# Performance work log

Hardware: AMD Instinct MI355X
Metric: run time of the kernel (lower is better)

## Reference

```python
import jax, jax.numpy as jnp
import numpy as np

ROUTINGS = 4
NUM_CAPSULE = 16
DIM_CAPSULE = 16
EPS = 1e-7  # K.epsilon()
L2_EPS = 1e-12  # tf.nn.l2_normalize epsilon


def squash(x, axis=-1):
    s = jnp.sum(jnp.square(x), axis=axis, keepdims=True) + EPS
    scale = jnp.sqrt(s) / (0.5 + s)
    return scale * x


def l2_normalize(x, axis=-1):
    s = jnp.sum(jnp.square(x), axis=axis, keepdims=True)
    return x * jax.lax.rsqrt(jnp.maximum(s, L2_EPS))


def setup_inputs() -> dict:
    key = jax.random.key(0)
    k1, k2 = jax.random.split(key)
    u_vecs = jax.random.normal(k1, (32, 4096, 128), dtype=jnp.float32)
    # glorot-ish scale for kernel-size-1 conv weight (input_dim=128 -> num_cap*dim_cap=256)
    W = jax.random.normal(k2, (128, 256), dtype=jnp.float32) * 0.05
    return {"u_vecs": u_vecs, "W": W}


def reference(u_vecs, W):
    B, I, _ = u_vecs.shape
    # conv1d with kernel size 1 == pointwise projection
    u_hat = jnp.einsum('bid,dk->bik', u_vecs, W)
    u_hat = u_hat.reshape(B, I, NUM_CAPSULE, DIM_CAPSULE)
    u_hat = jnp.transpose(u_hat, (0, 2, 1, 3))  # [B, N, I, D]

    b = jnp.zeros((B, NUM_CAPSULE, I), dtype=u_hat.dtype)
    o = None
    for i in range(ROUTINGS):
        c = jax.nn.softmax(b, axis=1)  # softmax over output-capsule axis
        o = jnp.einsum('bni,bnid->bnd', c, u_hat)  # [B, N, D]
        if i < ROUTINGS - 1:
            o = l2_normalize(o, axis=-1)
            b = jnp.einsum('bnd,bnid->bni', o, u_hat)  # logits reset each iter
    return squash(o, axis=-1)
```

## Files before the change

### kernel.cpp

```cpp
#include <hip/hip_runtime.h>

#define BATCH 32
#define I_TOT 4096
#define N_CAP 16
#define K_DIM 128
#define RCHUNK 128
#define NCHUNK 32
#define CCHUNK 64
#define NCHUNK_CS 64

#define WS_WO    0
#define WS_SP    65536
#define WS_PACK  2162688
#define WS_PACKT (WS_PACK + 8388608)
#define WS_TOTAL_F (WS_PACKT + 8388608)

typedef __attribute__((ext_vector_type(8))) short bf16x8;
typedef __attribute__((ext_vector_type(4))) float f32x4;

__device__ inline ushort f2bf(float x) {
    unsigned u = __float_as_uint(x);
    u += 0x7FFFu + ((u >> 16) & 1u);
    return (ushort)(u >> 16);
}

__global__ __launch_bounds__(256) void pack_kernel(const float* __restrict__ u,
                                                   float* __restrict__ ws, int do_pack) {
    const int b = blockIdx.y, chunk = blockIdx.x, t = threadIdx.x;
    const int c0 = chunk * CCHUNK;
    ushort* up = (ushort*)(ws + WS_PACK);
    ushort* ut = (ushort*)(ws + WS_PACKT);
    const int k4 = t & 31, rg = t >> 5;

    __shared__ ushort lds_bf[CCHUNK][K_DIM + 8];
    __shared__ __align__(16) float4 red[8][32];

    float4 acc = {0.f, 0.f, 0.f, 0.f};
    #pragma unroll
    for (int m = 0; m < 8; m++) {
        int R = c0 + m * 8 + rg;
        float4 v = *(const float4*)&u[((size_t)b * I_TOT + R) * K_DIM + k4 * 4];
        acc.x += v.x; acc.y += v.y; acc.z += v.z; acc.w += v.w;
        if (do_pack) {
            ushort4 w = { f2bf(v.x), f2bf(v.y), f2bf(v.z), f2bf(v.w) };
            int k = k4 * 4;
            int kt = k >> 5, lane_hi = (k & 31) >> 3, j0 = k & 7;
            size_t off = (((size_t)(b * 256 + (R >> 4)) * 4 + kt) * 64
                          + (R & 15) + (lane_hi << 4)) * 8 + j0;
            *(ushort4*)&up[off] = w;
            *(ushort4*)&lds_bf[m * 8 + rg][k] = w;
        }
    }
    red[rg][k4] = acc;
    __syncthreads();
    if (t < 32) {
        float4 s = red[0][t];
        #pragma unroll
        for (int r = 1; r < 8; r++) {
            float4 v = red[r][t];
            s.x += v.x; s.y += v.y; s.z += v.z; s.w += v.w;
        }
        *(float4*)&ws[WS_SP + ((size_t)(b * NCHUNK_CS + chunk)) * K_DIM + t * 4] = s;
    }

    if (do_pack) {
        __syncthreads();
        #pragma unroll
        for (int q = 0; q < 4; q++) {
            int cc = q * 256 + t;
            int k = cc & 127, io = cc >> 7;
            int ig0 = c0 + io * 8;
            bf16x8 w8;
            #pragma unroll
            for (int j = 0; j < 8; j++) w8[j] = (short)lds_bf[io * 8 + j][k];
            size_t off = ((((size_t)(b * 8 + (k >> 4))) * 128 + (ig0 >> 5)) * 64
                          + (k & 15) + ((io & 3) << 4)) * 8;
            *(bf16x8*)&ut[off] = w8;
        }
    }
}

__global__ __launch_bounds__(128) void update_kernel(const float* __restrict__ W,
                                                     float* __restrict__ ws,
                                                     float* __restrict__ out,
                                                     int mode) {
    const int n = blockIdx.x, b = blockIdx.y, t = threadIdx.x;

    __shared__ float s_n[K_DIM];
    __shared__ float o_s[N_CAP + 4];

    if (mode == 0) {
        const float* sp = ws + WS_SP + (size_t)b * NCHUNK_CS * K_DIM;
        float a = 0.f;
        #pragma unroll 8
        for (int c = 0; c < NCHUNK_CS; c++) a += sp[(size_t)c * K_DIM + t];
        s_n[t] = a * (1.f / 16.f);
    } else {
        const float* sp = ws + WS_SP + (size_t)b * NCHUNK * 2048 + n * K_DIM;
        float a = 0.f;
        #pragma unroll 8
        for (int c = 0; c < NCHUNK; c++) a += sp[(size_t)c * 2048 + t];
        s_n[t] = a;
    }
    __syncthreads();

    {
        const int d = t >> 3, kseg = t & 7;
        const int col = n * 16 + d;
        float p = 0.f;
        #pragma unroll
        for (int j = 0; j < 16; j++) {
            int k = kseg * 16 + j;
            p += s_n[k] * W[k * 256 + col];
        }
        p += __shfl_xor(p, 1); p += __shfl_xor(p, 2); p += __shfl_xor(p, 4);
        if (kseg == 0) o_s[d] = p;
    }
    __syncthreads();

    float ss = (mode == 2) ? 1e-7f : 0.f;
    #pragma unroll
    for (int d = 0; d < 16; d++) { float v = o_s[d]; ss += v * v; }

    if (mode == 2) {
        if (t < 16) {
            float scale = sqrtf(ss) / (0.5f + ss);
            out[b * 256 + n * 16 + t] = scale * o_s[t];
        }
        return;
    }

    const float inv = rsqrtf(fmaxf(ss, 1e-12f));
    const float4* wrow = (const float4*)(W + t * 256 + n * 16);
    const float4* o4 = (const float4*)o_s;
    float acc = 0.f;
    #pragma unroll
    for (int q = 0; q < 4; q++) {
        float4 w = wrow[q];
        float4 o = o4[q];
        acc += w.x * o.x + w.y * o.y + w.z * o.z + w.w * o.w;
    }
    ws[WS_WO + (size_t)b * 2048 + n * K_DIM + t] = acc * inv;
}

__global__ __launch_bounds__(256) void routing_mfma(float* __restrict__ ws) {
    const int b = blockIdx.y, chunk = blockIdx.x, t = threadIdx.x;
    const int lane = t & 63, wave = t >> 6;
    const short* up = (const short*)(ws + WS_PACK);
    const short* utp = (const short*)(ws + WS_PACKT);

    __shared__ __align__(16) short wo_bf[N_CAP][144];
    __shared__ float c_s[RCHUNK][18];

    const float* wo = ws + WS_WO + (size_t)b * 2048;
    #pragma unroll
    for (int j = 0; j < 8; j++) {
        int idx = t + j * 256;
        wo_bf[idx >> 7][idx & 127] = (short)f2bf(wo[idx]);
    }
    __syncthreads();

    const int cap = lane & 15, hi = lane >> 4;
    bf16x8 bfrag[4];
    #pragma unroll
    for (int kt = 0; kt < 4; kt++)
        bfrag[kt] = *(const bf16x8*)&wo_bf[cap][kt * 32 + hi * 8];

    #pragma unroll
    for (int rr = 0; rr < 2; rr++) {
        const int rt = wave * 2 + rr;
        const int rt_g = chunk * 8 + rt;
        f32x4 acc = {0.f, 0.f, 0.f, 0.f};
        const short* abase = up + (((size_t)(b * 256 + rt_g)) * 4) * 512 + lane * 8;
        #pragma unroll
        for (int kt = 0; kt < 4; kt++) {
            bf16x8 a = *(const bf16x8*)(abase + kt * 512);
            acc = __builtin_amdgcn_mfma_f32_16x16x32_bf16(a, bfrag[kt], acc, 0, 0, 0);
        }
        #pragma unroll
        for (int r = 0; r < 4; r++) {
            float v = acc[r];
            float mx = v;
            mx = fmaxf(mx, __shfl_xor(mx, 1)); mx = fmaxf(mx, __shfl_xor(mx, 2));
            mx = fmaxf(mx, __shfl_xor(mx, 4)); mx = fmaxf(mx, __shfl_xor(mx, 8));
            float e = __expf(v - mx);
            float sm = e;
            sm += __shfl_xor(sm, 1); sm += __shfl_xor(sm, 2);
            sm += __shfl_xor(sm, 4); sm += __shfl_xor(sm, 8);
            c_s[rt * 16 + hi * 4 + r][cap] = e / sm;
        }
    }
    __syncthreads();

    f32x4 s0 = {0.f, 0.f, 0.f, 0.f}, s1 = {0.f, 0.f, 0.f, 0.f};
    const size_t ut_b = ((size_t)b * 8) * 128;
    #pragma unroll
    for (int ic = 0; ic < 4; ic++) {
        bf16x8 bfr;
        #pragma unroll
        for (int j = 0; j < 8; j++)
            bfr[j] = (short)f2bf(c_s[ic * 32 + hi * 8 + j][cap]);
        const short* ab0 = utp + (((ut_b + (size_t)(wave * 2 + 0) * 128) + chunk * 4 + ic) * 64 + lane) * 8;
        const short* ab1 = utp + (((ut_b + (size_t)(wave * 2 + 1) * 128) + chunk * 4 + ic) * 64 + lane) * 8;
        bf16x8 a0 = *(const bf16x8*)ab0;
        bf16x8 a1 = *(const bf16x8*)ab1;
        s0 = __builtin_amdgcn_mfma_f32_16x16x32_bf16(a0, bfr, s0, 0, 0, 0);
        s1 = __builtin_amdgcn_mfma_f32_16x16x32_bf16(a1, bfr, s1, 0, 0, 0);
    }
    float* sp = ws + WS_SP + ((size_t)b * NCHUNK + chunk) * 2048;
    #pragma unroll
    for (int r = 0; r < 4; r++) {
        sp[cap * K_DIM + (wave * 2 + 0) * 16 + hi * 4 + r] = s0[r];
        sp[cap * K_DIM + (wave * 2 + 1) * 16 + hi * 4 + r] = s1[r];
    }
}

__global__ __launch_bounds__(256) void routing_fp32(const float* __restrict__ u,
                                                    float* __restrict__ ws) {
    const int b = blockIdx.y, chunk = blockIdx.x, t = threadIdx.x;
    const int i0 = chunk * RCHUNK;

    __shared__ __align__(16) float wo_s[N_CAP][K_DIM];
    __shared__ __align__(16) float c_s[RCHUNK][N_CAP];

    const float* w_o = ws + WS_WO + (size_t)b * 2048;
    #pragma unroll
    for (int j = 0; j < 8; j++) {
        int idx = t + j * 256;
        ((float*)wo_s)[idx] = w_o[idx];
    }
    __syncthreads();

    {
        const int row = t >> 1, h = t & 1;
        const float4* upx = (const float4*)(u + ((size_t)b * I_TOT + i0 + row) * K_DIM + h * 64);
        const float4* wp = (const float4*)&wo_s[0][h * 64];
        float logit[16];
        #pragma unroll
        for (int n = 0; n < 16; n++) logit[n] = 0.f;
        #pragma unroll
        for (int q = 0; q < 16; q++) {
            float4 v = upx[q];
            #pragma unroll
            for (int n = 0; n < 16; n++) {
                float4 w = wp[n * 32 + q];
                logit[n] += v.x * w.x + v.y * w.y + v.z * w.z + v.w * w.w;
            }
        }
        #pragma unroll
        for (int n = 0; n < 16; n++) logit[n] += __shfl_xor(logit[n], 1);
        float m = logit[0];
        #pragma unroll
        for (int n = 1; n < 16; n++) m = fmaxf(m, logit[n]);
        float sum = 0.f;
        #pragma unroll
        for (int n = 0; n < 16; n++) { logit[n] = __expf(logit[n] - m); sum += logit[n]; }
        float inv = 1.f / sum;
        float4* crow = (float4*)&c_s[row][h * 8];
        if (h == 0) {
            crow[0] = make_float4(logit[0]*inv, logit[1]*inv, logit[2]*inv, logit[3]*inv);
            crow[1] = make_float4(logit[4]*inv, logit[5]*inv, logit[6]*inv, logit[7]*inv);
        } else {
            crow[0] = make_float4(logit[8]*inv, logit[9]*inv, logit[10]*inv, logit[11]*inv);
            crow[1] = make_float4(logit[12]*inv, logit[13]*inv, logit[14]*inv, logit[15]*inv);
        }
    }
    __syncthreads();

    const int k4 = t & 31, ng = t >> 5;
    float4 a0 = {0.f,0.f,0.f,0.f}, a1 = {0.f,0.f,0.f,0.f};
    const float4* u2 = (const float4*)(u + ((size_t)b * I_TOT + i0) * K_DIM) + k4;
    #pragma unroll 8
    for (int i = 0; i < RCHUNK; i++) {
        float4 v = u2[(size_t)i * 32];
        float2 c2 = *(const float2*)&c_s[i][ng * 2];
        a0.x += v.x * c2.x; a0.y += v.y * c2.x; a0.z += v.z * c2.x; a0.w += v.w * c2.x;
        a1.x += v.x * c2.y; a1.y += v.y * c2.y; a1.z += v.z * c2.y; a1.w += v.w * c2.y;
    }
    float* sp = ws + WS_SP + ((size_t)b * NCHUNK + chunk) * 2048;
    *(float4*)&sp[(ng * 2 + 0) * K_DIM + k4 * 4] = a0;
    *(float4*)&sp[(ng * 2 + 1) * K_DIM + k4 * 4] = a1;
}

extern "C" void kernel_launch(void* const* d_in, const int* in_sizes, int n_in,
                              void* d_out, int out_size, void* d_ws, size_t ws_size,
                              hipStream_t stream) {
    const float* u = (const float*)d_in[0];
    const float* W = (const float*)d_in[1];
    float* out = (float*)d_out;
    float* ws = (float*)d_ws;

    const int big = (ws_size >= (size_t)WS_TOTAL_F * 4) ? 1 : 0;

    pack_kernel<<<dim3(I_TOT / CCHUNK, BATCH), 256, 0, stream>>>(u, ws, big);
    update_kernel<<<dim3(N_CAP, BATCH), 128, 0, stream>>>(W, ws, out, 0);

    for (int pass = 0; pass < 3; pass++) {
        if (big) routing_mfma<<<dim3(NCHUNK, BATCH), 256, 0, stream>>>(ws);
        else     routing_fp32<<<dim3(NCHUNK, BATCH), 256, 0, stream>>>(u, ws);
        update_kernel<<<dim3(N_CAP, BATCH), 128, 0, stream>>>(W, ws, out, pass == 2 ? 2 : 1);
    }
}
```

Before: 84.04 us.

## Fuse capsule update into routing kernel and double the per-block row chunk

Each routing block now reduces the previous pass's partial sums itself, projects them through W, normalizes, and builds the bf16 weighted-W tile, so the separate update kernel launches go away. Partial sums are double-buffered in the workspace so that this in-block reduction can read the prior pass while the current pass writes. The chunk size grows to 256 rows for both pack and routing, halving the grid and the number of partials. A small final kernel applies squash. The cost is that every block redundantly repeats the reduction and W projection for its batch, and the grid has fewer blocks.

```diff
diff --git a/kernel.cpp b/kernel.cpp
--- a/kernel.cpp
+++ b/kernel.cpp
@@ -4,16 +4,20 @@
 #define I_TOT 4096
 #define N_CAP 16
 #define K_DIM 128
-#define RCHUNK 128
-#define NCHUNK 32
-#define CCHUNK 64
-#define NCHUNK_CS 64
-
-#define WS_WO    0
+
+#define PCHUNK 256
+#define NPCH   16
+
+#define WS_CS    0
 #define WS_SP    65536
-#define WS_PACK  2162688
+#define WS_PACK  (WS_SP + 2097152)
 #define WS_PACKT (WS_PACK + 8388608)
 #define WS_TOTAL_F (WS_PACKT + 8388608)
+
+#define FB_WO   WS_PACK
+#define FB_SP   (WS_PACK + 65536)
+#define FB_NCHUNK 32
+#define RCHUNK 128
 
 typedef __attribute__((ext_vector_type(8))) short bf16x8;
 typedef __attribute__((ext_vector_type(4))) float f32x4;
@@ -27,28 +31,47 @@
 __global__ __launch_bounds__(256) void pack_kernel(const float* __restrict__ u,
                                                    float* __restrict__ ws, int do_pack) {
     const int b = blockIdx.y, chunk = blockIdx.x, t = threadIdx.x;
-    const int c0 = chunk * CCHUNK;
+    const int c0 = chunk * PCHUNK;
     ushort* up = (ushort*)(ws + WS_PACK);
     ushort* ut = (ushort*)(ws + WS_PACKT);
     const int k4 = t & 31, rg = t >> 5;
 
-    __shared__ ushort lds_bf[CCHUNK][K_DIM + 8];
+    __shared__ ushort lds_bf[64][K_DIM + 8];
     __shared__ __align__(16) float4 red[8][32];
 
     float4 acc = {0.f, 0.f, 0.f, 0.f};
-    #pragma unroll
-    for (int m = 0; m < 8; m++) {
-        int R = c0 + m * 8 + rg;
-        float4 v = *(const float4*)&u[((size_t)b * I_TOT + R) * K_DIM + k4 * 4];
-        acc.x += v.x; acc.y += v.y; acc.z += v.z; acc.w += v.w;
+    for (int slab = 0; slab < 4; slab++) {
+        const int s0 = c0 + slab * 64;
+        #pragma unroll
+        for (int m = 0; m < 8; m++) {
+            int R = s0 + m * 8 + rg;
+            float4 v = *(const float4*)&u[((size_t)b * I_TOT + R) * K_DIM + k4 * 4];
+            acc.x += v.x; acc.y += v.y; acc.z += v.z; acc.w += v.w;
+            if (do_pack) {
+                ushort4 w = { f2bf(v.x), f2bf(v.y), f2bf(v.z), f2bf(v.w) };
+                int k = k4 * 4;
+                int kt = k >> 5, lane_hi = (k & 31) >> 3, j0 = k & 7;
+                size_t off = (((size_t)(b * 256 + (R >> 4)) * 4 + kt) * 64
+                              + (R & 15) + (lane_hi << 4)) * 8 + j0;
+                *(ushort4*)&up[off] = w;
+                *(ushort4*)&lds_bf[m * 8 + rg][k] = w;
+            }
+        }
         if (do_pack) {
-            ushort4 w = { f2bf(v.x), f2bf(v.y), f2bf(v.z), f2bf(v.w) };
-            int k = k4 * 4;
-            int kt = k >> 5, lane_hi = (k & 31) >> 3, j0 = k & 7;
-            size_t off = (((size_t)(b * 256 + (R >> 4)) * 4 + kt) * 64
-                          + (R & 15) + (lane_hi << 4)) * 8 + j0;
-            *(ushort4*)&up[off] = w;
-            *(ushort4*)&lds_bf[m * 8 + rg][k] = w;
+            __syncthreads();
+            #pragma unroll
+            for (int q = 0; q < 4; q++) {
+                int cc = q * 256 + t;
+                int k = cc & 127, io = cc >> 7;
+                int ig0 = s0 + io * 8;
+                bf16x8 w8;
+                #pragma unroll
+                for (int j = 0; j < 8; j++) w8[j] = (short)lds_bf[io * 8 + j][k];
+                size_t off = ((((size_t)(b * 8 + (k >> 4))) * 128 + (ig0 >> 5)) * 64
+                              + (k & 15) + ((io & 3) << 4)) * 8;
+                *(bf16x8*)&ut[off] = w8;
+            }
+            __syncthreads();
         }
     }
     red[rg][k4] = acc;
@@ -60,103 +83,78 @@
             float4 v = red[r][t];
             s.x += v.x; s.y += v.y; s.z += v.z; s.w += v.w;
         }
-        *(float4*)&ws[WS_SP + ((size_t)(b * NCHUNK_CS + chunk)) * K_DIM + t * 4] = s;
-    }
-
-    if (do_pack) {
-        __syncthreads();
-        #pragma unroll
-        for (int q = 0; q < 4; q++) {
-            int cc = q * 256 + t;
-            int k = cc & 127, io = cc >> 7;
-            int ig0 = c0 + io * 8;
-            bf16x8 w8;
-            #pragma unroll
-            for (int j = 0; j < 8; j++) w8[j] = (short)lds_bf[io * 8 + j][k];
-            size_t off = ((((size_t)(b * 8 + (k >> 4))) * 128 + (ig0 >> 5)) * 64
-                          + (k & 15) + ((io & 3) << 4)) * 8;
-            *(bf16x8*)&ut[off] = w8;
-        }
-    }
-}
-
-__global__ __launch_bounds__(128) void update_kernel(const float* __restrict__ W,
-                                                     float* __restrict__ ws,
-                                                     float* __restrict__ out,
-                                                     int mode) {
-    const int n = blockIdx.x, b = blockIdx.y, t = threadIdx.x;
-
-    __shared__ float s_n[K_DIM];
-    __shared__ float o_s[N_CAP + 4];
-
-    if (mode == 0) {
-        const float* sp = ws + WS_SP + (size_t)b * NCHUNK_CS * K_DIM;
-        float a = 0.f;
-        #pragma unroll 8
-        for (int c = 0; c < NCHUNK_CS; c++) a += sp[(size_t)c * K_DIM + t];
-        s_n[t] = a * (1.f / 16.f);
-    } else {
-        const float* sp = ws + WS_SP + (size_t)b * NCHUNK * 2048 + n * K_DIM;
-        float a = 0.f;
-        #pragma unroll 8
-        for (int c = 0; c < NCHUNK; c++) a += sp[(size_t)c * 2048 + t];
-        s_n[t] = a;
-    }
-    __syncthreads();
-
-    {
-        const int d = t >> 3, kseg = t & 7;
-        const int col = n * 16 + d;
-        float p = 0.f;
-        #pragma unroll
-        for (int j = 0; j < 16; j++) {
-            int k = kseg * 16 + j;
-            p += s_n[k] * W[k * 256 + col];
-        }
-        p += __shfl_xor(p, 1); p += __shfl_xor(p, 2); p += __shfl_xor(p, 4);
-        if (kseg == 0) o_s[d] = p;
-    }
-    __syncthreads();
-
-    float ss = (mode == 2) ? 1e-7f : 0.f;
-    #pragma unroll
-    for (int d = 0; d < 16; d++) { float v = o_s[d]; ss += v * v; }
-
-    if (mode == 2) {
-        if (t < 16) {
-            float scale = sqrtf(ss) / (0.5f + ss);
-            out[b * 256 + n * 16 + t] = scale * o_s[t];
-        }
-        return;
-    }
-
-    const float inv = rsqrtf(fmaxf(ss, 1e-12f));
-    const float4* wrow = (const float4*)(W + t * 256 + n * 16);
-    const float4* o4 = (const float4*)o_s;
-    float acc = 0.f;
-    #pragma unroll
-    for (int q = 0; q < 4; q++) {
-        float4 w = wrow[q];
-        float4 o = o4[q];
-        acc += w.x * o.x + w.y * o.y + w.z * o.z + w.w * o.w;
-    }
-    ws[WS_WO + (size_t)b * 2048 + n * K_DIM + t] = acc * inv;
-}
-
-__global__ __launch_bounds__(256) void routing_mfma(float* __restrict__ ws) {
+        *(float4*)&ws[WS_CS + ((size_t)(b * NPCH + chunk)) * K_DIM + t * 4] = s;
+    }
+}
+
+__global__ __launch_bounds__(256) void routing_mfma(const float* __restrict__ W,
+                                                    float* __restrict__ ws,
+                                                    int pass) {
     const int b = blockIdx.y, chunk = blockIdx.x, t = threadIdx.x;
     const int lane = t & 63, wave = t >> 6;
     const short* up = (const short*)(ws + WS_PACK);
     const short* utp = (const short*)(ws + WS_PACKT);
 
-    __shared__ __align__(16) short wo_bf[N_CAP][144];
-    __shared__ float c_s[RCHUNK][18];
-
-    const float* wo = ws + WS_WO + (size_t)b * 2048;
+    __shared__ float s_lds[N_CAP * K_DIM];
+    __shared__ float o_lds[256];
+    __shared__ float on_lds[256];
+    __shared__ __align__(16) short wo_bf[N_CAP][136];
+    __shared__ __align__(16) ushort c_bf[N_CAP][264];
+
+    if (pass == 0) {
+        if (t < 128) {
+            const float* cs = ws + WS_CS + (size_t)b * NPCH * K_DIM;
+            float a = 0.f;
+            #pragma unroll
+            for (int c = 0; c < NPCH; c++) a += cs[c * K_DIM + t];
+            s_lds[t] = a * (1.f / 16.f);
+        }
+    } else {
+        const float4* spr = (const float4*)(ws + WS_SP + (size_t)b * 65536
+                                            + ((pass + 1) & 1) * 32768);
+        #pragma unroll
+        for (int j = 0; j < 2; j++) {
+            int f4 = t + j * 256;
+            float4 a = {0.f, 0.f, 0.f, 0.f};
+            #pragma unroll
+            for (int ch = 0; ch < NPCH; ch++) {
+                float4 v = spr[(size_t)ch * 512 + f4];
+                a.x += v.x; a.y += v.y; a.z += v.z; a.w += v.w;
+            }
+            *(float4*)&s_lds[f4 * 4] = a;
+        }
+    }
+    __syncthreads();
+
+    {
+        const float* srow = (pass == 0) ? s_lds : &s_lds[(t >> 4) * K_DIM];
+        float o = 0.f;
+        #pragma unroll 8
+        for (int k = 0; k < K_DIM; k++) o += srow[k] * W[k * 256 + t];
+        o_lds[t] = o;
+    }
+    __syncthreads();
+    {
+        int n = t >> 4;
+        float ss = 0.f;
+        #pragma unroll
+        for (int d = 0; d < 16; d++) { float v = o_lds[n * 16 + d]; ss += v * v; }
+        on_lds[t] = o_lds[t] * rsqrtf(fmaxf(ss, 1e-12f));
+    }
+    __syncthreads();
     #pragma unroll
     for (int j = 0; j < 8; j++) {
-        int idx = t + j * 256;
-        wo_bf[idx >> 7][idx & 127] = (short)f2bf(wo[idx]);
+        int e = t + j * 256;
+        int n2 = e >> 7, k = e & 127;
+        const float4* wr = (const float4*)(W + k * 256 + n2 * 16);
+        const float4* ov = (const float4*)&on_lds[n2 * 16];
+        float a = 0.f;
+        #pragma unroll
+        for (int q = 0; q < 4; q++) {
+            float4 w = wr[q], o4 = ov[q];
+            a += w.x * o4.x + w.y * o4.y + w.z * o4.z + w.w * o4.w;
+        }
+        wo_bf[n2][k] = (short)f2bf(a);
     }
     __syncthreads();
 
@@ -167,9 +165,9 @@
         bfrag[kt] = *(const bf16x8*)&wo_bf[cap][kt * 32 + hi * 8];
 
     #pragma unroll
-    for (int rr = 0; rr < 2; rr++) {
-        const int rt = wave * 2 + rr;
-        const int rt_g = chunk * 8 + rt;
+    for (int rr = 0; rr < 4; rr++) {
+        const int rt = wave * 4 + rr;
+        const int rt_g = chunk * NPCH + rt;
         f32x4 acc = {0.f, 0.f, 0.f, 0.f};
         const short* abase = up + (((size_t)(b * 256 + rt_g)) * 4) * 512 + lane * 8;
         #pragma unroll
@@ -187,32 +185,131 @@
             float sm = e;
             sm += __shfl_xor(sm, 1); sm += __shfl_xor(sm, 2);
             sm += __shfl_xor(sm, 4); sm += __shfl_xor(sm, 8);
-            c_s[rt * 16 + hi * 4 + r][cap] = e / sm;
+            c_bf[cap][rt * 16 + hi * 4 + r] = f2bf(e / sm);
         }
     }
     __syncthreads();
 
     f32x4 s0 = {0.f, 0.f, 0.f, 0.f}, s1 = {0.f, 0.f, 0.f, 0.f};
-    const size_t ut_b = ((size_t)b * 8) * 128;
-    #pragma unroll
-    for (int ic = 0; ic < 4; ic++) {
-        bf16x8 bfr;
-        #pragma unroll
-        for (int j = 0; j < 8; j++)
-            bfr[j] = (short)f2bf(c_s[ic * 32 + hi * 8 + j][cap]);
-        const short* ab0 = utp + (((ut_b + (size_t)(wave * 2 + 0) * 128) + chunk * 4 + ic) * 64 + lane) * 8;
-        const short* ab1 = utp + (((ut_b + (size_t)(wave * 2 + 1) * 128) + chunk * 4 + ic) * 64 + lane) * 8;
+    const size_t ut_b = (size_t)b * 8;
+    #pragma unroll
+    for (int ic = 0; ic < 8; ic++) {
+        bf16x8 bfr = *(const bf16x8*)&c_bf[cap][ic * 32 + hi * 8];
+        const size_t tile = (size_t)chunk * 8 + ic;
+        const short* ab0 = utp + (((ut_b + wave * 2 + 0) * 128 + tile) * 64 + lane) * 8;
+        const short* ab1 = utp + (((ut_b + wave * 2 + 1) * 128 + tile) * 64 + lane) * 8;
         bf16x8 a0 = *(const bf16x8*)ab0;
         bf16x8 a1 = *(const bf16x8*)ab1;
         s0 = __builtin_amdgcn_mfma_f32_16x16x32_bf16(a0, bfr, s0, 0, 0, 0);
         s1 = __builtin_amdgcn_mfma_f32_16x16x32_bf16(a1, bfr, s1, 0, 0, 0);
     }
-    float* sp = ws + WS_SP + ((size_t)b * NCHUNK + chunk) * 2048;
+    float* spw = ws + WS_SP + (size_t)b * 65536 + (pass & 1) * 32768 + chunk * 2048;
     #pragma unroll
     for (int r = 0; r < 4; r++) {
-        sp[cap * K_DIM + (wave * 2 + 0) * 16 + hi * 4 + r] = s0[r];
-        sp[cap * K_DIM + (wave * 2 + 1) * 16 + hi * 4 + r] = s1[r];
-    }
+        spw[cap * K_DIM + (wave * 2 + 0) * 16 + hi * 4 + r] = s0[r];
+        spw[cap * K_DIM + (wave * 2 + 1) * 16 + hi * 4 + r] = s1[r];
+    }
+}
+
+__global__ __launch_bounds__(256) void final_kernel(const float* __restrict__ W,
+                                                    float* __restrict__ ws,
+                                                    float* __restrict__ out) {
+    const int b = blockIdx.x, t = threadIdx.x;
+    __shared__ float s_lds[N_CAP * K_DIM];
+    __shared__ float o_lds[256];
+
+    const float4* spr = (const float4*)(ws + WS_SP + (size_t)b * 65536);
+    #pragma unroll
+    for (int j = 0; j < 2; j++) {
+        int f4 = t + j * 256;
+        float4 a = {0.f, 0.f, 0.f, 0.f};
+        #pragma unroll
+        for (int ch = 0; ch < NPCH; ch++) {
+            float4 v = spr[(size_t)ch * 512 + f4];
+            a.x += v.x; a.y += v.y; a.z += v.z; a.w += v.w;
+        }
+        *(float4*)&s_lds[f4 * 4] = a;
+    }
+    __syncthreads();
+
+    float o = 0.f;
+    {
+        const float* srow = &s_lds[(t >> 4) * K_DIM];
+        #pragma unroll 8
+        for (int k = 0; k < K_DIM; k++) o += srow[k] * W[k * 256 + t];
+        o_lds[t] = o;
+    }
+    __syncthreads();
+
+    const int n = t >> 4;
+    float ss = 1e-7f;
+    #pragma unroll
+    for (int d = 0; d < 16; d++) { float v = o_lds[n * 16 + d]; ss += v * v; }
+    float scale = sqrtf(ss) / (0.5f + ss);
+    out[b * 256 + t] = scale * o;
+}
+
+__global__ __launch_bounds__(128) void update_kernel(const float* __restrict__ W,
+                                                     float* __restrict__ ws,
+                                                     float* __restrict__ out,
+                                                     int mode) {
+    const int n = blockIdx.x, b = blockIdx.y, t = threadIdx.x;
+
+    __shared__ float s_n[K_DIM];
+    __shared__ float o_s[N_CAP + 4];
+
+    if (mode == 0) {
+        const float* sp = ws + WS_CS + (size_t)b * NPCH * K_DIM;
+        float a = 0.f;
+        #pragma unroll
+        for (int c = 0; c < NPCH; c++) a += sp[(size_t)c * K_DIM + t];
+        s_n[t] = a * (1.f / 16.f);
+    } else {
+        const float* sp = ws + FB_SP + (size_t)b * FB_NCHUNK * 2048 + n * K_DIM;
+        float a = 0.f;
+        #pragma unroll 8
+        for (int c = 0; c < FB_NCHUNK; c++) a += sp[(size_t)c * 2048 + t];
+        s_n[t] = a;
+    }
+    __syncthreads();
+
+    {
+        const int d = t >> 3, kseg = t & 7;
+        const int col = n * 16 + d;
+        float p = 0.f;
+        #pragma unroll
+        for (int j = 0; j < 16; j++) {
+            int k = kseg * 16 + j;
+            p += s_n[k] * W[k * 256 + col];
+        }
+        p += __shfl_xor(p, 1); p += __shfl_xor(p, 2); p += __shfl_xor(p, 4);
+        if (kseg == 0) o_s[d] = p;
+    }
+    __syncthreads();
+
+    float ss = (mode == 2) ? 1e-7f : 0.f;
+    #pragma unroll
+    for (int d = 0; d < 16; d++) { float v = o_s[d]; ss += v * v; }
+
+    if (mode == 2) {
+        if (t < 16) {
+            float scale = sqrtf(ss) / (0.5f + ss);
+            out[b * 256 + n * 16 + t] = scale * o_s[t];
+        }
+        return;
+    }
+
+    const float inv = rsqrtf(fmaxf(ss, 1e-12f));
+    const float4* wrow = (const float4*)(W + t * 256 + n * 16);
+    const float4* o4 = (const float4*)o_s;
+    float acc = 0.f;
+    #pragma unroll
+    for (int q = 0; q < 4; q++) {
+        float4 w = wrow[q];
+        float4 o = o4[q];
+        acc += w.x * o.x + w.y * o.y + w.z * o.z + w.w * o.w;
+    }
+    ws[FB_WO + (size_t)b * 2048 + n * K_DIM + t] = acc * inv;
 }
 
 __global__ __launch_bounds__(256) void routing_fp32(const float* __restrict__ u,
@@ -223,7 +320,7 @@
     __shared__ __align__(16) float wo_s[N_CAP][K_DIM];
     __shared__ __align__(16) float c_s[RCHUNK][N_CAP];
 
-    const float* w_o = ws + WS_WO + (size_t)b * 2048;
+    const float* w_o = ws + FB_WO + (size_t)b * 2048;
     #pragma unroll
     for (int j = 0; j < 8; j++) {
         int idx = t + j * 256;
@@ -277,7 +374,7 @@
         a0.x += v.x * c2.x; a0.y += v.y * c2.x; a0.z += v.z * c2.x; a0.w += v.w * c2.x;
         a1.x += v.x * c2.y; a1.y += v.y * c2.y; a1.z += v.z * c2.y; a1.w += v.w * c2.y;
     }
-    float* sp = ws + WS_SP + ((size_t)b * NCHUNK + chunk) * 2048;
+    float* sp = ws + FB_SP + ((size_t)b * FB_NCHUNK + chunk) * 2048;
     *(float4*)&sp[(ng * 2 + 0) * K_DIM + k4 * 4] = a0;
     *(float4*)&sp[(ng * 2 + 1) * K_DIM + k4 * 4] = a1;
 }
@@ -292,12 +389,17 @@
 
     const int big = (ws_size >= (size_t)WS_TOTAL_F * 4) ? 1 : 0;
 
-    pack_kernel<<<dim3(I_TOT / CCHUNK, BATCH), 256, 0, stream>>>(u, ws, big);
-    update_kernel<<<dim3(N_CAP, BATCH), 128, 0, stream>>>(W, ws, out, 0);
-
-    for (int pass = 0; pass < 3; pass++) {
-        if (big) routing_mfma<<<dim3(NCHUNK, BATCH), 256, 0, stream>>>(ws);
-        else     routing_fp32<<<dim3(NCHUNK, BATCH), 256, 0, stream>>>(u, ws);
-        update_kernel<<<dim3(N_CAP, BATCH), 128, 0, stream>>>(W, ws, out, pass == 2 ? 2 : 1);
-    }
-}
+    pack_kernel<<<dim3(NPCH, BATCH), 256, 0, stream>>>(u, ws, big);
+
+    if (big) {
+        for (int pass = 0; pass < 3; pass++)
+            routing_mfma<<<dim3(NPCH, BATCH), 256, 0, stream>>>(W, ws, pass);
+        final_kernel<<<BATCH, 256, 0, stream>>>(W, ws, out);
+    } else {
+        update_kernel<<<dim3(N_CAP, BATCH), 128, 0, stream>>>(W, ws, out, 0);
+        for (int pass = 0; pass < 3; pass++) {
+            routing_fp32<<<dim3(FB_NCHUNK, BATCH), 256, 0, stream>>>(u, ws);
+            update_kernel<<<dim3(N_CAP, BATCH), 128, 0, stream>>>(W, ws, out, pass == 2 ? 2 : 1);
+        }
+    }
+}
```

New measurement: 110.0 us. 30.9% more time.

## Drop row-major bf16 pack; read fp32 input directly in routing logits stage

Applied to the files above, without the earlier changes.

The pack kernel no longer writes a separate MFMA-layout bf16 copy of the input, so it only writes the transposed copy. The routing kernel now loads fp32 rows of the input and converts them to bf16 in registers for the logit MFMA. The update kernel writes the normalized weight-output vector directly in bf16, so routing loads it with one vector read instead of converting per element. Coupling coefficients are kept as bf16 in shared memory in the transposed layout, so the second MFMA reads a fragment with one vector load. This removes a 16 MB write and drops the pack read from the routing passes. The trade is reading 32 MB of fp32 per routing pass instead of 16 MB of bf16, and adding per-pass conversion work.

```diff
diff --git a/kernel.cpp b/kernel.cpp
--- a/kernel.cpp
+++ b/kernel.cpp
@@ -4,15 +4,17 @@
 #define I_TOT 4096
 #define N_CAP 16
 #define K_DIM 128
+
+#define CCHUNK 64
+#define NCH_CS 64
+#define NRCH 32
 #define RCHUNK 128
-#define NCHUNK 32
-#define CCHUNK 64
-#define NCHUNK_CS 64
-
-#define WS_WO    0
-#define WS_SP    65536
-#define WS_PACK  2162688
-#define WS_PACKT (WS_PACK + 8388608)
+
+#define WS_CS    0
+#define WS_FBWO  262144
+#define WS_WOB   327680
+#define WS_SP    360448
+#define WS_PACKT 2457600
 #define WS_TOTAL_F (WS_PACKT + 8388608)
 
 typedef __attribute__((ext_vector_type(8))) short bf16x8;
@@ -28,7 +30,6 @@
                                                    float* __restrict__ ws, int do_pack) {
     const int b = blockIdx.y, chunk = blockIdx.x, t = threadIdx.x;
     const int c0 = chunk * CCHUNK;
-    ushort* up = (ushort*)(ws + WS_PACK);
     ushort* ut = (ushort*)(ws + WS_PACKT);
     const int k4 = t & 31, rg = t >> 5;
 
@@ -43,12 +44,7 @@
         acc.x += v.x; acc.y += v.y; acc.z += v.z; acc.w += v.w;
         if (do_pack) {
             ushort4 w = { f2bf(v.x), f2bf(v.y), f2bf(v.z), f2bf(v.w) };
-            int k = k4 * 4;
-            int kt = k >> 5, lane_hi = (k & 31) >> 3, j0 = k & 7;
-            size_t off = (((size_t)(b * 256 + (R >> 4)) * 4 + kt) * 64
-                          + (R & 15) + (lane_hi << 4)) * 8 + j0;
-            *(ushort4*)&up[off] = w;
-            *(ushort4*)&lds_bf[m * 8 + rg][k] = w;
+            *(ushort4*)&lds_bf[m * 8 + rg][k4 * 4] = w;
         }
     }
     red[rg][k4] = acc;
@@ -60,7 +56,7 @@
             float4 v = red[r][t];
             s.x += v.x; s.y += v.y; s.z += v.z; s.w += v.w;
         }
-        *(float4*)&ws[WS_SP + ((size_t)(b * NCHUNK_CS + chunk)) * K_DIM + t * 4] = s;
+        *(float4*)&ws[WS_CS + ((size_t)(b * NCH_CS + chunk)) * K_DIM + t * 4] = s;
     }
 
     if (do_pack) {
@@ -83,23 +79,23 @@
 __global__ __launch_bounds__(128) void update_kernel(const float* __restrict__ W,
                                                      float* __restrict__ ws,
                                                      float* __restrict__ out,
-                                                     int mode) {
+                                                     int mode, int wo_bf16) {
     const int n = blockIdx.x, b = blockIdx.y, t = threadIdx.x;
 
     __shared__ float s_n[K_DIM];
     __shared__ float o_s[N_CAP + 4];
 
     if (mode == 0) {
-        const float* sp = ws + WS_SP + (size_t)b * NCHUNK_CS * K_DIM;
+        const float* cs = ws + WS_CS + (size_t)b * NCH_CS * K_DIM;
+        float a = 0.f;
+        #pragma unroll 16
+        for (int c = 0; c < NCH_CS; c++) a += cs[(size_t)c * K_DIM + t];
+        s_n[t] = a * (1.f / 16.f);
+    } else {
+        const float* sp = ws + WS_SP + (size_t)b * NRCH * 2048 + n * K_DIM;
         float a = 0.f;
         #pragma unroll 8
-        for (int c = 0; c < NCHUNK_CS; c++) a += sp[(size_t)c * K_DIM + t];
-        s_n[t] = a * (1.f / 16.f);
-    } else {
-        const float* sp = ws + WS_SP + (size_t)b * NCHUNK * 2048 + n * K_DIM;
-        float a = 0.f;
-        #pragma unroll 8
-        for (int c = 0; c < NCHUNK; c++) a += sp[(size_t)c * 2048 + t];
+        for (int c = 0; c < NRCH; c++) a += sp[(size_t)c * 2048 + t];
         s_n[t] = a;
     }
     __syncthreads();
@@ -140,23 +136,26 @@
         float4 o = o4[q];
         acc += w.x * o.x + w.y * o.y + w.z * o.z + w.w * o.w;
     }
-    ws[WS_WO + (size_t)b * 2048 + n * K_DIM + t] = acc * inv;
-}
-
-__global__ __launch_bounds__(256) void routing_mfma(float* __restrict__ ws) {
+    if (wo_bf16) {
+        ((ushort*)(ws + WS_WOB))[(size_t)b * 2048 + n * K_DIM + t] = f2bf(acc * inv);
+    } else {
+        ws[WS_FBWO + (size_t)b * 2048 + n * K_DIM + t] = acc * inv;
+    }
+}
+
+__global__ __launch_bounds__(256) void routing_mfma(const float* __restrict__ u,
+                                                    float* __restrict__ ws) {
     const int b = blockIdx.y, chunk = blockIdx.x, t = threadIdx.x;
     const int lane = t & 63, wave = t >> 6;
-    const short* up = (const short*)(ws + WS_PACK);
     const short* utp = (const short*)(ws + WS_PACKT);
 
     __shared__ __align__(16) short wo_bf[N_CAP][144];
-    __shared__ float c_s[RCHUNK][18];
-
-    const float* wo = ws + WS_WO + (size_t)b * 2048;
-    #pragma unroll
-    for (int j = 0; j < 8; j++) {
-        int idx = t + j * 256;
-        wo_bf[idx >> 7][idx & 127] = (short)f2bf(wo[idx]);
+    __shared__ __align__(16) ushort c_bf[N_CAP][264];
+
+    {
+        const ushort* wob = (const ushort*)(ws + WS_WOB) + (size_t)b * 2048;
+        bf16x8 v = *(const bf16x8*)&wob[t * 8];
+        *(bf16x8*)&wo_bf[t >> 4][(t & 15) * 8] = v;
     }
     __syncthreads();
 
@@ -169,12 +168,18 @@
     #pragma unroll
     for (int rr = 0; rr < 2; rr++) {
         const int rt = wave * 2 + rr;
-        const int rt_g = chunk * 8 + rt;
+        const int row = chunk * RCHUNK + rt * 16 + cap;
+        const float* ubase = u + ((size_t)b * I_TOT + row) * K_DIM + hi * 8;
         f32x4 acc = {0.f, 0.f, 0.f, 0.f};
-        const short* abase = up + (((size_t)(b * 256 + rt_g)) * 4) * 512 + lane * 8;
         #pragma unroll
         for (int kt = 0; kt < 4; kt++) {
-            bf16x8 a = *(const bf16x8*)(abase + kt * 512);
+            float4 f0 = *(const float4*)(ubase + kt * 32);
+            float4 f1 = *(const float4*)(ubase + kt * 32 + 4);
+            bf16x8 a;
+            a[0] = (short)f2bf(f0.x); a[1] = (short)f2bf(f0.y);
+            a[2] = (short)f2bf(f0.z); a[3] = (short)f2bf(f0.w);
+            a[4] = (short)f2bf(f1.x); a[5] = (short)f2bf(f1.y);
+            a[6] = (short)f2bf(f1.z); a[7] = (short)f2bf(f1.w);
             acc = __builtin_amdgcn_mfma_f32_16x16x32_bf16(a, bfrag[kt], acc, 0, 0, 0);
         }
         #pragma unroll
@@ -187,31 +192,29 @@
             float sm = e;
             sm += __shfl_xor(sm, 1); sm += __shfl_xor(sm, 2);
             sm += __shfl_xor(sm, 4); sm += __shfl_xor(sm, 8);
-            c_s[rt * 16 + hi * 4 + r][cap] = e / sm;
+            c_bf[cap][rt * 16 + hi * 4 + r] = f2bf(e / sm);
         }
     }
     __syncthreads();
 
     f32x4 s0 = {0.f, 0.f, 0.f, 0.f}, s1 = {0.f, 0.f, 0.f, 0.f};
-    const size_t ut_b = ((size_t)b * 8) * 128;
+    const size_t ut_b = (size_t)b * 8;
     #pragma unroll
     for (int ic = 0; ic < 4; ic++) {
-        bf16x8 bfr;
-        #pragma unroll
-        for (int j = 0; j < 8; j++)
-            bfr[j] = (short)f2bf(c_s[ic * 32 + hi * 8 + j][cap]);
-        const short* ab0 = utp + (((ut_b + (size_t)(wave * 2 + 0) * 128) + chunk * 4 + ic) * 64 + lane) * 8;
-        const short* ab1 = utp + (((ut_b + (size_t)(wave * 2 + 1) * 128) + chunk * 4 + ic) * 64 + lane) * 8;
+        bf16x8 bfr = *(const bf16x8*)&c_bf[cap][ic * 32 + hi * 8];
+        const size_t tile = (size_t)chunk * 4 + ic;
+        const short* ab0 = utp + (((ut_b + wave * 2 + 0) * 128 + tile) * 64 + lane) * 8;
+        const short* ab1 = utp + (((ut_b + wave * 2 + 1) * 128 + tile) * 64 + lane) * 8;
         bf16x8 a0 = *(const bf16x8*)ab0;
         bf16x8 a1 = *(const bf16x8*)ab1;
         s0 = __builtin_amdgcn_mfma_f32_16x16x32_bf16(a0, bfr, s0, 0, 0, 0);
         s1 = __builtin_amdgcn_mfma_f32_16x16x32_bf16(a1, bfr, s1, 0, 0, 0);
     }
-    float* sp = ws + WS_SP + ((size_t)b * NCHUNK + chunk) * 2048;
+    float* spw = ws + WS_SP + ((size_t)b * NRCH + chunk) * 2048;
     #pragma unroll
     for (int r = 0; r < 4; r++) {
-        sp[cap * K_DIM + (wave * 2 + 0) * 16 + hi * 4 + r] = s0[r];
-        sp[cap * K_DIM + (wave * 2 + 1) * 16 + hi * 4 + r] = s1[r];
+        spw[cap * K_DIM + (wave * 2 + 0) * 16 + hi * 4 + r] = s0[r];
+        spw[cap * K_DIM + (wave * 2 + 1) * 16 + hi * 4 + r] = s1[r];
     }
 }
 
@@ -223,7 +226,7 @@
     __shared__ __align__(16) float wo_s[N_CAP][K_DIM];
     __shared__ __align__(16) float c_s[RCHUNK][N_CAP];
 
-    const float* w_o = ws + WS_WO + (size_t)b * 2048;
+    const float* w_o = ws + WS_FBWO + (size_t)b * 2048;
     #pragma unroll
     for (int j = 0; j < 8; j++) {
         int idx = t + j * 256;
@@ -277,7 +280,7 @@
         a0.x += v.x * c2.x; a0.y += v.y * c2.x; a0.z += v.z * c2.x; a0.w += v.w * c2.x;
         a1.x += v.x * c2.y; a1.y += v.y * c2.y; a1.z += v.z * c2.y; a1.w += v.w * c2.y;
     }
-    float* sp = ws + WS_SP + ((size_t)b * NCHUNK + chunk) * 2048;
+    float* sp = ws + WS_SP + ((size_t)b * NRCH + chunk) * 2048;
     *(float4*)&sp[(ng * 2 + 0) * K_DIM + k4 * 4] = a0;
     *(float4*)&sp[(ng * 2 + 1) * K_DIM + k4 * 4] = a1;
 }
@@ -292,12 +295,13 @@
 
     const int big = (ws_size >= (size_t)WS_TOTAL_F * 4) ? 1 : 0;
 
-    pack_kernel<<<dim3(I_TOT / CCHUNK, BATCH), 256, 0, stream>>>(u, ws, big);
-    update_kernel<<<dim3(N_CAP, BATCH), 128, 0, stream>>>(W, ws, out, 0);
+    pack_kernel<<<dim3(NCH_CS, BATCH), 256, 0, stream>>>(u, ws, big);
+    update_kernel<<<dim3(N_CAP, BATCH), 128, 0, stream>>>(W, ws, out, 0, big);
 
     for (int pass = 0; pass < 3; pass++) {
-        if (big) routing_mfma<<<dim3(NCHUNK, BATCH), 256, 0, stream>>>(ws);
-        else     routing_fp32<<<dim3(NCHUNK, BATCH), 256, 0, stream>>>(u, ws);
-        update_kernel<<<dim3(N_CAP, BATCH), 128, 0, stream>>>(W, ws, out, pass == 2 ? 2 : 1);
-    }
-}
+        if (big) routing_mfma<<<dim3(NRCH, BATCH), 256, 0, stream>>>(u, ws);
+        else     routing_fp32<<<dim3(NRCH, BATCH), 256, 0, stream>>>(u, ws);
+        update_kernel<<<dim3(N_CAP, BATCH), 128, 0, stream>>>(
+            W, ws, out, pass == 2 ? 2 : 1, big);
+    }
+}
```

Result: slower. 91.56 us (+8.9%).
